# Optimization experiments

Measured on AMD Instinct MI355X. Metric: run time of the kernel, lower is better.

Reference implementation:

```python
import jax, jax.numpy as jnp
import numpy as np

INPUT_DIM = 1024
LATENT_DIM = 256
NUM_EMB = 8192
BATCH = 8192


def setup_inputs() -> dict:
    key = jax.random.key(0)
    ks = jax.random.split(key, 6)
    x = jax.random.normal(ks[0], (BATCH, INPUT_DIM), dtype=jnp.float32)
    # torch nn.Linear stores weight as [out, in]
    enc_w = jax.random.normal(ks[1], (LATENT_DIM, INPUT_DIM), dtype=jnp.float32) / np.sqrt(INPUT_DIM)
    enc_b = jnp.zeros((LATENT_DIM,), dtype=jnp.float32)
    # embeddings initialized uniform(-1/K, 1/K) as in the module
    emb = jax.random.uniform(ks[2], (NUM_EMB, LATENT_DIM), dtype=jnp.float32,
                             minval=-1.0 / NUM_EMB, maxval=1.0 / NUM_EMB)
    dec_w = jax.random.normal(ks[3], (INPUT_DIM, LATENT_DIM), dtype=jnp.float32) / np.sqrt(LATENT_DIM)
    dec_b = jnp.zeros((INPUT_DIM,), dtype=jnp.float32)
    return {"x": x, "enc_w": enc_w, "enc_b": enc_b, "emb": emb,
            "dec_w": dec_w, "dec_b": dec_b}


def reference(x, enc_w, enc_b, emb, dec_w, dec_b):
    # encoder: z = x @ W_e^T + b_e  -> [B, D]
    z = x @ enc_w.T + enc_b
    # cosine distance to codebook: d = 1 - <z, e> / (||z|| ||e||)  -> [B, K]
    z_norm = jnp.linalg.norm(z, axis=1, keepdims=True)          # [B, 1]
    e_norm = jnp.linalg.norm(emb, axis=1)                        # [K]
    d = 1.0 - (z @ emb.T) / (z_norm * e_norm)
    idx = jnp.argmin(d, axis=1)                                  # [B]
    # one-hot @ codebook == direct gather of nearest code vectors
    z_q = jnp.take(emb, idx, axis=0)                             # [B, D]
    # straight-through: decoder input z + stop_grad(z_q - z)
    dec_in = z + jax.lax.stop_gradient(z_q - z)
    x_recon = dec_in @ dec_w.T + dec_b
    return (x_recon, z, z_q, idx.astype(jnp.int32))
```

## Files before the change

kernel.cpp:

```cpp
#include <hip/hip_runtime.h>
#include <math.h>

#define BATCH   8192
#define IN_DIM  1024
#define LAT     256
#define NEMB    8192

#define TAU 3.5e-3f

#define RESC_R 16

#define CSPLIT 16

typedef _Float16 f16x8 __attribute__((ext_vector_type(8)));
typedef _Float16 f16x4 __attribute__((ext_vector_type(4)));
typedef float f32x16_t __attribute__((ext_vector_type(16)));

typedef __attribute__((address_space(1))) const unsigned int gu32_t;
typedef __attribute__((address_space(3))) unsigned int lu32_t;

__device__ __forceinline__ unsigned int ford(float x) {
  unsigned int u = __float_as_uint(x);
  return (u & 0x80000000u) ? ~u : (u | 0x80000000u);
}
__device__ __forceinline__ float funord(unsigned int t) {
  unsigned int u = (t & 0x80000000u) ? (t & 0x7FFFFFFFu) : ~t;
  return __uint_as_float(u);
}

__global__ __launch_bounds__(256) void emb_prep(
    const float* __restrict__ emb, float* __restrict__ inv_norm,
    _Float16* __restrict__ efrag) {
  __shared__ float s_inv[32];
  const int tid = threadIdx.x;
  const int l = tid & 63;
  const int w = tid >> 6;
  const int tile = blockIdx.x;

  {
    int row = tid >> 3, part = tid & 7;
    const float* p = emb + (size_t)(tile * 32 + row) * 256 + part * 32;
    float s = 0.f;
#pragma unroll
    for (int j = 0; j < 8; ++j) {
      float4 v = *(const float4*)&p[4 * j];
      s += v.x * v.x + v.y * v.y + v.z * v.z + v.w * v.w;
    }
    s += __shfl_xor(s, 1);
    s += __shfl_xor(s, 2);
    s += __shfl_xor(s, 4);
    if (part == 0) {
      float iv = 1.0f / sqrtf(s);
      s_inv[row] = iv;
      inv_norm[tile * 32 + row] = iv;
    }
  }
  __syncthreads();

#pragma unroll
  for (int q = 0; q < 4; ++q) {
    int kb = w * 4 + q;
    int row = l & 31;
    int k = kb * 16 + (l >> 5) * 8;
    const float* p = emb + (size_t)(tile * 32 + row) * 256 + k;
    float sc = s_inv[row];
    f16x8 h;
#pragma unroll
    for (int j = 0; j < 8; ++j) h[j] = (_Float16)(p[j] * sc);
    size_t o = ((size_t)(tile * 16 + kb) * 64 + l) * 8;
    *(f16x8*)(efrag + o) = h;
  }
}

__device__ __forceinline__ void split_body(
    const float* __restrict__ src, _Float16* __restrict__ dst, size_t lo_off,
    int KD, int write_lo, int gw, int l) {
  int tile = gw / KD, kb = gw % KD;
  int row = tile * 32 + (l & 31);
  int k = kb * 16 + (l >> 5) * 8;
  const float* p = src + (size_t)row * (KD * 16) + k;
  f16x8 h, lo;
#pragma unroll
  for (int j = 0; j < 8; ++j) {
    float v = p[j];
    _Float16 hh = (_Float16)v;
    h[j] = hh;
    lo[j] = (_Float16)(v - (float)hh);
  }
  size_t o = ((size_t)gw * 64 + l) * 8;
  *(f16x8*)(dst + o) = h;
  if (write_lo) *(f16x8*)(dst + lo_off + o) = lo;
}

__global__ __launch_bounds__(256) void split16(
    const float* __restrict__ src, _Float16* __restrict__ dst, size_t lo_off,
    int KD, int write_lo) {
  int gw = (blockIdx.x * 256 + threadIdx.x) >> 6;
  split_body(src, dst, lo_off, KD, write_lo, gw, threadIdx.x & 63);
}

__global__ __launch_bounds__(256) void split_weights(
    const float* __restrict__ enc_w, _Float16* __restrict__ wfrag,
    const float* __restrict__ dec_w, _Float16* __restrict__ dwfrag) {
  int b = blockIdx.x;
  int l = threadIdx.x & 63;
  if (b < 128) {
    int gw = (b * 256 + threadIdx.x) >> 6;
    split_body(enc_w, wfrag, (size_t)LAT * IN_DIM, IN_DIM / 16, 1, gw, l);
  } else {
    int gw = ((b - 128) * 256 + threadIdx.x) >> 6;
    split_body(dec_w, dwfrag, (size_t)IN_DIM * LAT, LAT / 16, 1, gw, l);
  }
}

__global__ __launch_bounds__(256) void gemm16_frag(
    const _Float16* __restrict__ Afrag, size_t a_lo_off,
    const _Float16* __restrict__ Bfrag, size_t b_lo_off,
    const float* __restrict__ bias, float* __restrict__ C, int N, int K) {
  __shared__ char lds[32768];
  const int tid = threadIdx.x;
  const int l = tid & 63;
  const int w = tid >> 6;
  const int mt = w & 1, nt = w >> 1;
  const int rb = blockIdx.y * 64, cb = blockIdx.x * 64;
  const int KD = K >> 4;

  f32x16_t acc = (f32x16_t)0.0f;

  for (int s = 0; s < (K >> 6); ++s) {
#pragma unroll
    for (int i = 0; i < 8; ++i) {
      int c = i * 4 + w;
      int isB = c >> 4;
      int cc = c & 15;
      int t32 = cc >> 3, prec = (cc >> 2) & 1, ks = cc & 3;
      int tile = ((isB ? cb : rb) >> 5) + t32;
      int kb = s * 4 + ks;
      const _Float16* base = isB ? Bfrag : Afrag;
      size_t lo = isB ? b_lo_off : a_lo_off;
      const _Float16* src =
          base + (size_t)prec * lo + ((size_t)(tile * KD + kb) * 64 + l) * 8;
      __builtin_amdgcn_global_load_lds((gu32_t*)src,
                                       (lu32_t*)(lds + (c << 10) + l * 16),
                                       16, 0, 0);
    }
    __syncthreads();
#pragma unroll
    for (int ks = 0; ks < 4; ++ks) {
      f16x8 ah = *(const f16x8*)(lds + ((mt * 8 + ks) << 10) + l * 16);
      f16x8 al = *(const f16x8*)(lds + ((mt * 8 + 4 + ks) << 10) + l * 16);
      f16x8 bh = *(const f16x8*)(lds + 16384 + ((nt * 8 + ks) << 10) + l * 16);
      f16x8 bl = *(const f16x8*)(lds + 16384 + ((nt * 8 + 4 + ks) << 10) + l * 16);
      acc = __builtin_amdgcn_mfma_f32_32x32x16_f16(ah, bh, acc, 0, 0, 0);
      acc = __builtin_amdgcn_mfma_f32_32x32x16_f16(ah, bl, acc, 0, 0, 0);
      acc = __builtin_amdgcn_mfma_f32_32x32x16_f16(al, bh, acc, 0, 0, 0);
    }
    __syncthreads();
  }

  int col = cb + nt * 32 + (l & 31);
  float bv = bias[col];
#pragma unroll
  for (int r = 0; r < 16; ++r) {
    int row = rb + mt * 32 + (r & 3) + 8 * (r >> 2) + 4 * (l >> 5);
    C[(size_t)row * N + col] = acc[r] + bv;
  }
}

__global__ __launch_bounds__(256) void gemm16(
    const float* __restrict__ A, const _Float16* __restrict__ Bfrag,
    size_t b_lo_off, const float* __restrict__ bias, float* __restrict__ C,
    int M, int N, int K) {
  __shared__ char lds[32768];
  const int tid = threadIdx.x;
  const int l = tid & 63;
  const int w = tid >> 6;
  const int mt = w & 1, nt = w >> 1;
  const int rb = blockIdx.y * 64, cb = blockIdx.x * 64;
  const int KD = K >> 4;

  f32x16_t acc = (f32x16_t)0.0f;

  for (int s = 0; s < (K >> 6); ++s) {
#pragma unroll
    for (int i = 0; i < 4; ++i) {
      int c = i * 4 + w;
      int bnt = c >> 3, prec = (c >> 2) & 1, ks = c & 3;
      int tile = (cb >> 5) + bnt, ksg = s * 4 + ks;
      const _Float16* src = Bfrag + (size_t)prec * b_lo_off +
                            ((size_t)(tile * KD + ksg) * 64 + l) * 8;
      __builtin_amdgcn_global_load_lds((gu32_t*)src,
                                       (lu32_t*)(lds + 16384 + (c << 10) + l * 16),
                                       16, 0, 0);
    }
#pragma unroll
    for (int t = 0; t < 4; ++t) {
      int flat = t * 256 + tid;
      int r = flat >> 4, c4 = flat & 15;
      float4 v = *(const float4*)&A[(size_t)(rb + r) * K + s * 64 + 4 * c4];
      int kk = 4 * c4;
      int ks = kk >> 4, j = kk & 7;
      int lane2 = (r & 31) + 32 * ((kk >> 3) & 1);
      int mtt = r >> 5;
      f16x4 hv, lv;
      float vv[4] = {v.x, v.y, v.z, v.w};
#pragma unroll
      for (int e = 0; e < 4; ++e) {
        _Float16 h = (_Float16)vv[e];
        hv[e] = h;
        lv[e] = (_Float16)(vv[e] - (float)h);
      }
      int base = ((mtt * 8 + ks) << 10) + lane2 * 16 + j * 2;
      *(f16x4*)(lds + base) = hv;
      *(f16x4*)(lds + base + 4096) = lv;
    }
    __syncthreads();
#pragma unroll
    for (int ks = 0; ks < 4; ++ks) {
      f16x8 ah = *(const f16x8*)(lds + ((mt * 8 + ks) << 10) + l * 16);
      f16x8 al = *(const f16x8*)(lds + ((mt * 8 + 4 + ks) << 10) + l * 16);
      f16x8 bh = *(const f16x8*)(lds + 16384 + ((nt * 8 + ks) << 10) + l * 16);
      f16x8 bl = *(const f16x8*)(lds + 16384 + ((nt * 8 + 4 + ks) << 10) + l * 16);
      acc = __builtin_amdgcn_mfma_f32_32x32x16_f16(ah, bh, acc, 0, 0, 0);
      acc = __builtin_amdgcn_mfma_f32_32x32x16_f16(ah, bl, acc, 0, 0, 0);
      acc = __builtin_amdgcn_mfma_f32_32x32x16_f16(al, bh, acc, 0, 0, 0);
    }
    __syncthreads();
  }

  int col = cb + nt * 32 + (l & 31);
  float bv = bias[col];
#pragma unroll
  for (int r = 0; r < 16; ++r) {
    int row = rb + mt * 32 + (r & 3) + 8 * (r >> 2) + 4 * (l >> 5);
    C[(size_t)row * N + col] = acc[r] + bv;
  }
}

__global__ __launch_bounds__(256) void gemm16_dec(
    const int* __restrict__ idxi, const unsigned int* __restrict__ flags,
    const unsigned long long* __restrict__ packed_rescore,
    const float* __restrict__ emb, const _Float16* __restrict__ Bfrag,
    size_t b_lo_off, const float* __restrict__ bias, float* __restrict__ C,
    float* __restrict__ zq, float* __restrict__ idx_out) {
  __shared__ char lds[32768];
  __shared__ int idxs[64];
  const int tid = threadIdx.x;
  const int l = tid & 63;
  const int w = tid >> 6;
  const int mt = w & 1, nt = w >> 1;
  const int rb = blockIdx.y * 64, cb = blockIdx.x * 64;
  const int KD = 16;

  if (tid < 64) {
    int row = rb + tid;
    int idx = idxi[row];
    if (flags[row]) idx = NEMB - 1 - (int)(packed_rescore[row] & 0xFFFFFFFFull);
    idxs[tid] = idx;
    if (blockIdx.x == 0) idx_out[row] = (float)idx;
  }
  __syncthreads();

  f32x16_t acc = (f32x16_t)0.0f;

  for (int s = 0; s < 4; ++s) {
#pragma unroll
    for (int i = 0; i < 4; ++i) {
      int c = i * 4 + w;
      int bnt = c >> 3, prec = (c >> 2) & 1, ks = c & 3;
      int tile = (cb >> 5) + bnt, ksg = s * 4 + ks;
      const _Float16* src = Bfrag + (size_t)prec * b_lo_off +
                            ((size_t)(tile * KD + ksg) * 64 + l) * 8;
      __builtin_amdgcn_global_load_lds((gu32_t*)src,
                                       (lu32_t*)(lds + 16384 + (c << 10) + l * 16),
                                       16, 0, 0);
    }
#pragma unroll
    for (int t = 0; t < 4; ++t) {
      int flat = t * 256 + tid;
      int r = flat >> 4, c4 = flat & 15;
      float4 v = *(const float4*)&emb[(size_t)idxs[r] * 256 + s * 64 + 4 * c4];
      if (blockIdx.x == 0)
        *(float4*)&zq[(size_t)(rb + r) * 256 + s * 64 + 4 * c4] = v;
      int kk = 4 * c4;
      int ks = kk >> 4, j = kk & 7;
      int lane2 = (r & 31) + 32 * ((kk >> 3) & 1);
      int mtt = r >> 5;
      f16x4 hv, lv;
      float vv[4] = {v.x, v.y, v.z, v.w};
#pragma unroll
      for (int e = 0; e < 4; ++e) {
        _Float16 h = (_Float16)vv[e];
        hv[e] = h;
        lv[e] = (_Float16)(vv[e] - (float)h);
      }
      int base = ((mtt * 8 + ks) << 10) + lane2 * 16 + j * 2;
      *(f16x4*)(lds + base) = hv;
      *(f16x4*)(lds + base + 4096) = lv;
    }
    __syncthreads();
#pragma unroll
    for (int ks = 0; ks < 4; ++ks) {
      f16x8 ah = *(const f16x8*)(lds + ((mt * 8 + ks) << 10) + l * 16);
      f16x8 al = *(const f16x8*)(lds + ((mt * 8 + 4 + ks) << 10) + l * 16);
      f16x8 bh = *(const f16x8*)(lds + 16384 + ((nt * 8 + ks) << 10) + l * 16);
      f16x8 bl = *(const f16x8*)(lds + 16384 + ((nt * 8 + 4 + ks) << 10) + l * 16);
      acc = __builtin_amdgcn_mfma_f32_32x32x16_f16(ah, bh, acc, 0, 0, 0);
      acc = __builtin_amdgcn_mfma_f32_32x32x16_f16(ah, bl, acc, 0, 0, 0);
      acc = __builtin_amdgcn_mfma_f32_32x32x16_f16(al, bh, acc, 0, 0, 0);
    }
    __syncthreads();
  }

  int col = cb + nt * 32 + (l & 31);
  float bv = bias[col];
#pragma unroll
  for (int r = 0; r < 16; ++r) {
    int row = rb + mt * 32 + (r & 3) + 8 * (r >> 2) + 4 * (l >> 5);
    C[(size_t)row * IN_DIM + col] = acc[r] + bv;
  }
}

__global__ __launch_bounds__(256) void score_mfma(
    const _Float16* __restrict__ zfrag, const _Float16* __restrict__ efrag,
    unsigned long long* __restrict__ cand1, unsigned int* __restrict__ cand2) {
  __shared__ char lds[32768];
  const int tid = threadIdx.x;
  const int l = tid & 63;
  const int w = tid >> 6;
  const int csplit = blockIdx.x;
  const int rowgrp = blockIdx.y;

  f16x8 a[16];
  {
    const _Float16* ab =
        zfrag + (((size_t)(rowgrp * 4 + w) * 16) * 64 + l) * 8;
#pragma unroll
    for (int kf = 0; kf < 16; ++kf)
      a[kf] = *(const f16x8*)(ab + (size_t)kf * 512);
  }

  float b1[16], b2[16];
  int i1[16];
#pragma unroll
  for (int r = 0; r < 16; ++r) {
    b1[r] = -INFINITY;
    b2[r] = -INFINITY;
    i1[r] = 0;
  }

  const char* esrc = (const char*)efrag + (size_t)csplit * 262144 + tid * 16;
  char* ldst = lds + tid * 16;
  const char* ldsr = lds + l * 16;

#pragma unroll
  for (int i = 0; i < 4; ++i)
    __builtin_amdgcn_global_load_lds((gu32_t*)(esrc + i * 4096),
                                     (lu32_t*)(ldst + i * 4096), 16, 0, 0);

#pragma unroll 1
  for (int p = 0; p < 16; ++p) {
    asm volatile("s_waitcnt vmcnt(0)" ::: "memory");
    __builtin_amdgcn_s_barrier();
    __builtin_amdgcn_sched_barrier(0);

    if (p < 15) {
      const char* sb = esrc + (size_t)(p + 1) * 16384;
      char* db = ldst + ((p + 1) & 1) * 16384;
#pragma unroll
      for (int i = 0; i < 4; ++i)
        __builtin_amdgcn_global_load_lds((gu32_t*)(sb + i * 4096),
                                         (lu32_t*)(db + i * 4096), 16, 0, 0);
    }

    const char* bb = ldsr + (p & 1) * 16384;
    f32x16_t acc0 = (f32x16_t)0.0f;
    f32x16_t acc1 = (f32x16_t)0.0f;
#pragma unroll
    for (int kb = 0; kb < 16; kb += 2) {
      f16x8 bh0 = *(const f16x8*)(bb + (kb << 10));
      f16x8 bh1 = *(const f16x8*)(bb + ((kb + 1) << 10));
      acc0 = __builtin_amdgcn_mfma_f32_32x32x16_f16(a[kb], bh0, acc0, 0, 0, 0);
      acc1 = __builtin_amdgcn_mfma_f32_32x32x16_f16(a[kb + 1], bh1, acc1, 0, 0, 0);
    }

    const int col = csplit * 512 + p * 32 + (l & 31);
#pragma unroll
    for (int r = 0; r < 16; ++r) {
      float v = acc0[r] + acc1[r];
      float nb2 = __builtin_amdgcn_fmed3f(v, b1[r], b2[r]);
      if (v > b1[r]) i1[r] = col;
      b1[r] = fmaxf(b1[r], v);
      b2[r] = nb2;
    }
  }

#pragma unroll
  for (int r = 0; r < 16; ++r) {
    float v1 = b1[r], v2 = b2[r];
    int vi = i1[r];
#pragma unroll
    for (int m = 1; m < 32; m <<= 1) {
      float o1 = __shfl_xor(v1, m);
      int oi = __shfl_xor(vi, m);
      float o2 = __shfl_xor(v2, m);
      float n2v = fmaxf(fminf(v1, o1), fmaxf(v2, o2));
      if (o1 > v1 || (o1 == v1 && oi < vi)) {
        v1 = o1;
        vi = oi;
      }
      v2 = n2v;
    }
    if ((l & 31) == 0) {
      int row = rowgrp * 128 + w * 32 + (r & 3) + 8 * (r >> 2) + 4 * (l >> 5);
      cand1[(size_t)row * CSPLIT + csplit] =
          ((unsigned long long)ford(v1) << 32) |
          (unsigned long long)(unsigned int)(NEMB - 1 - vi);
      cand2[(size_t)row * CSPLIT + csplit] = ford(v2);
    }
  }
}

__global__ __launch_bounds__(256) void finalize1(
    const unsigned long long* __restrict__ cand1,
    const unsigned int* __restrict__ cand2, int* __restrict__ idxi,
    unsigned int* __restrict__ flags, unsigned int* __restrict__ flag_count,
    unsigned int* __restrict__ flag_list) {
  int row = blockIdx.x * 256 + threadIdx.x;
  unsigned long long best = 0;
  unsigned int second = 0;
  int bslot = 0;
#pragma unroll
  for (int s = 0; s < CSPLIT; ++s) {
    unsigned long long v = cand1[(size_t)row * CSPLIT + s];
    unsigned int vs = (unsigned int)(v >> 32);
    if (v > best) {
      second = (unsigned int)(best >> 32);
      best = v;
      bslot = s;
    } else if (vs > second) {
      second = vs;
    }
  }
  unsigned int r2 = cand2[(size_t)row * CSPLIT + bslot];
  if (r2 > second) second = r2;
  float s1 = funord((unsigned int)(best >> 32));
  float s2 = funord(second);
  int idx = NEMB - 1 - (int)(best & 0xFFFFFFFFull);
  idxi[row] = idx;
  unsigned int fl = ((s1 - s2) < TAU) ? 1u : 0u;
  flags[row] = fl;
  if (fl) {
    unsigned int p = atomicAdd(flag_count, 1u);
    flag_list[p] = row;
  }
}

__global__ __launch_bounds__(256) void rescore(
    const float* __restrict__ z, const float* __restrict__ emb,
    const float* __restrict__ inv_norm,
    const unsigned int* __restrict__ flag_list,
    const unsigned int* __restrict__ flag_count,
    unsigned long long* __restrict__ packed_rescore) {
  __shared__ float z_s[2][292];
  __shared__ unsigned long long red[64];
  const int tid = threadIdx.x;
  const int l = tid & 63;
  const int w = tid >> 6;
  const int cl = l & 7;
  const int p = l >> 3;
  const int code = w * 8 + cl;
  const int cbase = blockIdx.x * 32;
  const unsigned int rc = blockIdx.y;

  unsigned int cnt = *flag_count;
  if (2 * rc >= cnt) return;

  float4 e4[8];
  const float* ebase = emb + (size_t)(cbase + code) * 256 + p * 32;
#pragma unroll
  for (int j = 0; j < 8; ++j) e4[j] = *(const float4*)&ebase[4 * j];
  const float inv = inv_norm[cbase + code];
  const unsigned int lowbits = (unsigned int)(NEMB - 1 - (cbase + code));

  for (unsigned int f = 2 * rc; f < cnt; f += 2 * RESC_R) {
    int row0 = (int)flag_list[f];
    int row1 = (f + 1 < cnt) ? (int)flag_list[f + 1] : row0;
    __syncthreads();
    if (tid < 128) {
      int half = tid >> 6, t = tid & 63;
      int k0 = t * 4;
      int addr = k0 + 4 * (k0 >> 5);
      const float* zp = z + (size_t)(half ? row1 : row0) * 256 + k0;
      *(float4*)&z_s[half][addr] = *(const float4*)zp;
    }
    __syncthreads();
    float a0 = 0.f, a1 = 0.f;
#pragma unroll
    for (int j = 0; j < 8; ++j) {
      float4 z0 = *(const float4*)&z_s[0][p * 36 + 4 * j];
      float4 z1 = *(const float4*)&z_s[1][p * 36 + 4 * j];
      a0 += e4[j].x * z0.x + e4[j].y * z0.y + e4[j].z * z0.z + e4[j].w * z0.w;
      a1 += e4[j].x * z1.x + e4[j].y * z1.y + e4[j].z * z1.z + e4[j].w * z1.w;
    }
#pragma unroll
    for (int m = 8; m < 64; m <<= 1) {
      a0 += __shfl_xor(a0, m);
      a1 += __shfl_xor(a1, m);
    }
    if (l < 8)
      red[w * 8 + cl] = ((unsigned long long)ford(a0 * inv) << 32) | lowbits;
    else if (l < 16)
      red[32 + w * 8 + cl] = ((unsigned long long)ford(a1 * inv) << 32) | lowbits;
    __syncthreads();
    if (w == 0) {
      unsigned long long v = red[l];
#pragma unroll
      for (int m = 1; m < 32; m <<= 1) {
        unsigned long long o = __shfl_xor(v, m);
        if (o > v) v = o;
      }
      if (l == 0) atomicMax(&packed_rescore[row0], v);
      if (l == 32) atomicMax(&packed_rescore[row1], v);
    }
  }
}

extern "C" void kernel_launch(void* const* d_in, const int* in_sizes, int n_in,
                              void* d_out, int out_size, void* d_ws,
                              size_t ws_size, hipStream_t stream) {
  (void)in_sizes; (void)n_in; (void)out_size;
  const float* x     = (const float*)d_in[0];
  const float* enc_w = (const float*)d_in[1];
  const float* enc_b = (const float*)d_in[2];
  const float* emb   = (const float*)d_in[3];
  const float* dec_w = (const float*)d_in[4];
  const float* dec_b = (const float*)d_in[5];

  float* out     = (float*)d_out;
  float* x_recon = out;
  float* z_out   = x_recon + (size_t)BATCH * IN_DIM;
  float* zq_out  = z_out + (size_t)BATCH * LAT;
  float* idx_out = zq_out + (size_t)BATCH * LAT;

  char* ws = (char*)d_ws;
  float* inv_norm = (float*)ws;
  unsigned int* flags = (unsigned int*)(ws + 32768);
  int* idxi = (int*)(ws + 65536);
  unsigned int* flag_count = (unsigned int*)(ws + 98304);
  unsigned long long* packed_rescore =
      (unsigned long long*)(ws + 98432);
  unsigned int* flag_list = (unsigned int*)(ws + 163968);
  _Float16* wfrag  = (_Float16*)(ws + 1048576);
  _Float16* dwfrag = (_Float16*)(ws + 2097152);
  _Float16* efrag  = (_Float16*)(ws + 3145728);
  _Float16* zfrag  = (_Float16*)(ws + 7340032);
  unsigned long long* cand1 = (unsigned long long*)(ws + 11534336);
  unsigned int* cand2 = (unsigned int*)(ws + 12582912);
  _Float16* xfrag  = (_Float16*)(ws + 24117248);

  const bool has_x = ws_size >= 57671680ull;

  hipMemsetAsync(ws + 98304, 0, 128 + 65536, stream);

  emb_prep<<<NEMB / 32, 256, 0, stream>>>(emb, inv_norm, efrag);
  split_weights<<<256, 256, 0, stream>>>(enc_w, wfrag, dec_w, dwfrag);

  if (has_x) {
    split16<<<4096, 256, 0, stream>>>(x, xfrag, (size_t)BATCH * IN_DIM,
                                      IN_DIM / 16, 1);
    gemm16_frag<<<dim3(LAT / 64, BATCH / 64), 256, 0, stream>>>(
        xfrag, (size_t)BATCH * IN_DIM, wfrag, (size_t)LAT * IN_DIM, enc_b,
        z_out, LAT, IN_DIM);
  } else {
    gemm16<<<dim3(LAT / 64, BATCH / 64), 256, 0, stream>>>(
        x, wfrag, (size_t)LAT * IN_DIM, enc_b, z_out, BATCH, LAT, IN_DIM);
  }

  split16<<<1024, 256, 0, stream>>>(z_out, zfrag, (size_t)BATCH * LAT,
                                    LAT / 16, 0);

  score_mfma<<<dim3(CSPLIT, 64), 256, 0, stream>>>(zfrag, efrag, cand1, cand2);

  finalize1<<<32, 256, 0, stream>>>(cand1, cand2, idxi, flags, flag_count,
                                    flag_list);
  rescore<<<dim3(256, RESC_R), 256, 0, stream>>>(
      z_out, emb, inv_norm, flag_list, flag_count, packed_rescore);

  gemm16_dec<<<dim3(IN_DIM / 64, BATCH / 64), 256, 0, stream>>>(
      idxi, flags, packed_rescore, emb, dwfrag, (size_t)IN_DIM * LAT, dec_b,
      x_recon, zq_out, idx_out);
}
```

Before: 261.8 us.

## Triple-buffer codebook tiles in score kernel and drop pre-split x path

The scoring kernel moves from double to triple buffering of codebook tiles in LDS, prefetching two stages ahead with a partial vmcnt wait, so global-to-LDS loads overlap more with the MFMA work. It also raises wave priority around the MFMA loop. Separately, the encoder path that first split x into fp16 hi/lo fragments and then ran a fragment GEMM is removed, and gemm16 now reads x directly. This saves a full pass over x but may make the encoder GEMM less efficient, and the larger LDS footprint can lower occupancy.

```diff
diff --git a/kernel.cpp b/kernel.cpp
--- a/kernel.cpp
+++ b/kernel.cpp
@@ -110,60 +110,6 @@
   } else {
     int gw = ((b - 128) * 256 + threadIdx.x) >> 6;
     split_body(dec_w, dwfrag, (size_t)IN_DIM * LAT, LAT / 16, 1, gw, l);
-  }
-}
-
-__global__ __launch_bounds__(256) void gemm16_frag(
-    const _Float16* __restrict__ Afrag, size_t a_lo_off,
-    const _Float16* __restrict__ Bfrag, size_t b_lo_off,
-    const float* __restrict__ bias, float* __restrict__ C, int N, int K) {
-  __shared__ char lds[32768];
-  const int tid = threadIdx.x;
-  const int l = tid & 63;
-  const int w = tid >> 6;
-  const int mt = w & 1, nt = w >> 1;
-  const int rb = blockIdx.y * 64, cb = blockIdx.x * 64;
-  const int KD = K >> 4;
-
-  f32x16_t acc = (f32x16_t)0.0f;
-
-  for (int s = 0; s < (K >> 6); ++s) {
-#pragma unroll
-    for (int i = 0; i < 8; ++i) {
-      int c = i * 4 + w;
-      int isB = c >> 4;
-      int cc = c & 15;
-      int t32 = cc >> 3, prec = (cc >> 2) & 1, ks = cc & 3;
-      int tile = ((isB ? cb : rb) >> 5) + t32;
-      int kb = s * 4 + ks;
-      const _Float16* base = isB ? Bfrag : Afrag;
-      size_t lo = isB ? b_lo_off : a_lo_off;
-      const _Float16* src =
-          base + (size_t)prec * lo + ((size_t)(tile * KD + kb) * 64 + l) * 8;
-      __builtin_amdgcn_global_load_lds((gu32_t*)src,
-                                       (lu32_t*)(lds + (c << 10) + l * 16),
-                                       16, 0, 0);
-    }
-    __syncthreads();
-#pragma unroll
-    for (int ks = 0; ks < 4; ++ks) {
-      f16x8 ah = *(const f16x8*)(lds + ((mt * 8 + ks) << 10) + l * 16);
-      f16x8 al = *(const f16x8*)(lds + ((mt * 8 + 4 + ks) << 10) + l * 16);
-      f16x8 bh = *(const f16x8*)(lds + 16384 + ((nt * 8 + ks) << 10) + l * 16);
-      f16x8 bl = *(const f16x8*)(lds + 16384 + ((nt * 8 + 4 + ks) << 10) + l * 16);
-      acc = __builtin_amdgcn_mfma_f32_32x32x16_f16(ah, bh, acc, 0, 0, 0);
-      acc = __builtin_amdgcn_mfma_f32_32x32x16_f16(ah, bl, acc, 0, 0, 0);
-      acc = __builtin_amdgcn_mfma_f32_32x32x16_f16(al, bh, acc, 0, 0, 0);
-    }
-    __syncthreads();
-  }
-
-  int col = cb + nt * 32 + (l & 31);
-  float bv = bias[col];
-#pragma unroll
-  for (int r = 0; r < 16; ++r) {
-    int row = rb + mt * 32 + (r & 3) + 8 * (r >> 2) + 4 * (l >> 5);
-    C[(size_t)row * N + col] = acc[r] + bv;
   }
 }
 
@@ -324,7 +270,7 @@
 __global__ __launch_bounds__(256) void score_mfma(
     const _Float16* __restrict__ zfrag, const _Float16* __restrict__ efrag,
     unsigned long long* __restrict__ cand1, unsigned int* __restrict__ cand2) {
-  __shared__ char lds[32768];
+  __shared__ char lds[49152];
   const int tid = threadIdx.x;
   const int l = tid & 63;
   const int w = tid >> 6;
@@ -350,32 +296,45 @@
   }
 
   const char* esrc = (const char*)efrag + (size_t)csplit * 262144 + tid * 16;
-  char* ldst = lds + tid * 16;
-  const char* ldsr = lds + l * 16;
+
+  char* bc = lds;
+  char* bn = lds + 16384;
+  char* bf = lds + 32768;
 
 #pragma unroll
   for (int i = 0; i < 4; ++i)
     __builtin_amdgcn_global_load_lds((gu32_t*)(esrc + i * 4096),
-                                     (lu32_t*)(ldst + i * 4096), 16, 0, 0);
+                                     (lu32_t*)(bc + tid * 16 + i * 4096),
+                                     16, 0, 0);
+#pragma unroll
+  for (int i = 0; i < 4; ++i)
+    __builtin_amdgcn_global_load_lds((gu32_t*)(esrc + 16384 + i * 4096),
+                                     (lu32_t*)(bn + tid * 16 + i * 4096),
+                                     16, 0, 0);
 
 #pragma unroll 1
   for (int p = 0; p < 16; ++p) {
-    asm volatile("s_waitcnt vmcnt(0)" ::: "memory");
+    if (p < 15) {
+      asm volatile("s_waitcnt vmcnt(4)" ::: "memory");
+    } else {
+      asm volatile("s_waitcnt vmcnt(0)" ::: "memory");
+    }
     __builtin_amdgcn_s_barrier();
     __builtin_amdgcn_sched_barrier(0);
 
-    if (p < 15) {
-      const char* sb = esrc + (size_t)(p + 1) * 16384;
-      char* db = ldst + ((p + 1) & 1) * 16384;
+    if (p < 14) {
+      const char* sb = esrc + (size_t)(p + 2) * 16384;
 #pragma unroll
       for (int i = 0; i < 4; ++i)
         __builtin_amdgcn_global_load_lds((gu32_t*)(sb + i * 4096),
-                                         (lu32_t*)(db + i * 4096), 16, 0, 0);
-    }
-
-    const char* bb = ldsr + (p & 1) * 16384;
+                                         (lu32_t*)(bf + tid * 16 + i * 4096),
+                                         16, 0, 0);
+    }
+
+    const char* bb = bc + l * 16;
     f32x16_t acc0 = (f32x16_t)0.0f;
     f32x16_t acc1 = (f32x16_t)0.0f;
+    __builtin_amdgcn_s_setprio(1);
 #pragma unroll
     for (int kb = 0; kb < 16; kb += 2) {
       f16x8 bh0 = *(const f16x8*)(bb + (kb << 10));
@@ -383,6 +342,7 @@
       acc0 = __builtin_amdgcn_mfma_f32_32x32x16_f16(a[kb], bh0, acc0, 0, 0, 0);
       acc1 = __builtin_amdgcn_mfma_f32_32x32x16_f16(a[kb + 1], bh1, acc1, 0, 0, 0);
     }
+    __builtin_amdgcn_s_setprio(0);
 
     const int col = csplit * 512 + p * 32 + (l & 31);
 #pragma unroll
@@ -393,6 +353,11 @@
       b1[r] = fmaxf(b1[r], v);
       b2[r] = nb2;
     }
+
+    char* t = bc;
+    bc = bn;
+    bn = bf;
+    bf = t;
   }
 
 #pragma unroll
@@ -529,7 +494,7 @@
 extern "C" void kernel_launch(void* const* d_in, const int* in_sizes, int n_in,
                               void* d_out, int out_size, void* d_ws,
                               size_t ws_size, hipStream_t stream) {
-  (void)in_sizes; (void)n_in; (void)out_size;
+  (void)in_sizes; (void)n_in; (void)out_size; (void)ws_size;
   const float* x     = (const float*)d_in[0];
   const float* enc_w = (const float*)d_in[1];
   const float* enc_b = (const float*)d_in[2];
@@ -557,25 +522,14 @@
   _Float16* zfrag  = (_Float16*)(ws + 7340032);
   unsigned long long* cand1 = (unsigned long long*)(ws + 11534336);
   unsigned int* cand2 = (unsigned int*)(ws + 12582912);
-  _Float16* xfrag  = (_Float16*)(ws + 24117248);
-
-  const bool has_x = ws_size >= 57671680ull;
 
   hipMemsetAsync(ws + 98304, 0, 128 + 65536, stream);
 
   emb_prep<<<NEMB / 32, 256, 0, stream>>>(emb, inv_norm, efrag);
   split_weights<<<256, 256, 0, stream>>>(enc_w, wfrag, dec_w, dwfrag);
 
-  if (has_x) {
-    split16<<<4096, 256, 0, stream>>>(x, xfrag, (size_t)BATCH * IN_DIM,
-                                      IN_DIM / 16, 1);
-    gemm16_frag<<<dim3(LAT / 64, BATCH / 64), 256, 0, stream>>>(
-        xfrag, (size_t)BATCH * IN_DIM, wfrag, (size_t)LAT * IN_DIM, enc_b,
-        z_out, LAT, IN_DIM);
-  } else {
-    gemm16<<<dim3(LAT / 64, BATCH / 64), 256, 0, stream>>>(
-        x, wfrag, (size_t)LAT * IN_DIM, enc_b, z_out, BATCH, LAT, IN_DIM);
-  }
+  gemm16<<<dim3(LAT / 64, BATCH / 64), 256, 0, stream>>>(
+      x, wfrag, (size_t)LAT * IN_DIM, enc_b, z_out, BATCH, LAT, IN_DIM);
 
   split16<<<1024, 256, 0, stream>>>(z_out, zfrag, (size_t)BATCH * LAT,
                                     LAT / 16, 0);
```

Result: slower. 281.2 us (+7.4%).

## Fuse z fp16 conversion into scoring kernel and triple-buffer codebook loads

Applied to the files above, without the earlier changes.

The separate split16 pass that converted z to fp16 fragments is removed, and the scoring kernel now reads fp32 z directly and converts it in registers. The codebook staging in LDS goes from double to triple buffering with a prefetch distance of two, using a partial vmcnt wait. s_setprio is raised around the MFMA loop. This saves one kernel launch and a round trip of z through memory, and hides more load latency. The cost is larger LDS use, which may lower occupancy, plus uncoalesced fp32 loads of z per lane.

```diff
diff --git a/kernel.cpp b/kernel.cpp
--- a/kernel.cpp
+++ b/kernel.cpp
@@ -322,9 +322,9 @@
 }
 
 __global__ __launch_bounds__(256) void score_mfma(
-    const _Float16* __restrict__ zfrag, const _Float16* __restrict__ efrag,
+    const float* __restrict__ z, const _Float16* __restrict__ efrag,
     unsigned long long* __restrict__ cand1, unsigned int* __restrict__ cand2) {
-  __shared__ char lds[32768];
+  __shared__ char lds[49152];
   const int tid = threadIdx.x;
   const int l = tid & 63;
   const int w = tid >> 6;
@@ -333,11 +333,19 @@
 
   f16x8 a[16];
   {
-    const _Float16* ab =
-        zfrag + (((size_t)(rowgrp * 4 + w) * 16) * 64 + l) * 8;
-#pragma unroll
-    for (int kf = 0; kf < 16; ++kf)
-      a[kf] = *(const f16x8*)(ab + (size_t)kf * 512);
+    const float* zb =
+        z + (size_t)(rowgrp * 128 + w * 32 + (l & 31)) * 256 + (l >> 5) * 8;
+#pragma unroll
+    for (int kf = 0; kf < 16; ++kf) {
+      float4 v0 = *(const float4*)(zb + kf * 16);
+      float4 v1 = *(const float4*)(zb + kf * 16 + 4);
+      f16x8 h;
+      h[0] = (_Float16)v0.x; h[1] = (_Float16)v0.y;
+      h[2] = (_Float16)v0.z; h[3] = (_Float16)v0.w;
+      h[4] = (_Float16)v1.x; h[5] = (_Float16)v1.y;
+      h[6] = (_Float16)v1.z; h[7] = (_Float16)v1.w;
+      a[kf] = h;
+    }
   }
 
   float b1[16], b2[16];
@@ -350,32 +358,45 @@
   }
 
   const char* esrc = (const char*)efrag + (size_t)csplit * 262144 + tid * 16;
-  char* ldst = lds + tid * 16;
-  const char* ldsr = lds + l * 16;
+
+  char* bc = lds;
+  char* bn = lds + 16384;
+  char* bf = lds + 32768;
 
 #pragma unroll
   for (int i = 0; i < 4; ++i)
     __builtin_amdgcn_global_load_lds((gu32_t*)(esrc + i * 4096),
-                                     (lu32_t*)(ldst + i * 4096), 16, 0, 0);
+                                     (lu32_t*)(bc + tid * 16 + i * 4096),
+                                     16, 0, 0);
+#pragma unroll
+  for (int i = 0; i < 4; ++i)
+    __builtin_amdgcn_global_load_lds((gu32_t*)(esrc + 16384 + i * 4096),
+                                     (lu32_t*)(bn + tid * 16 + i * 4096),
+                                     16, 0, 0);
 
 #pragma unroll 1
   for (int p = 0; p < 16; ++p) {
-    asm volatile("s_waitcnt vmcnt(0)" ::: "memory");
+    if (p < 15) {
+      asm volatile("s_waitcnt vmcnt(4)" ::: "memory");
+    } else {
+      asm volatile("s_waitcnt vmcnt(0)" ::: "memory");
+    }
     __builtin_amdgcn_s_barrier();
     __builtin_amdgcn_sched_barrier(0);
 
-    if (p < 15) {
-      const char* sb = esrc + (size_t)(p + 1) * 16384;
-      char* db = ldst + ((p + 1) & 1) * 16384;
+    if (p < 14) {
+      const char* sb = esrc + (size_t)(p + 2) * 16384;
 #pragma unroll
       for (int i = 0; i < 4; ++i)
         __builtin_amdgcn_global_load_lds((gu32_t*)(sb + i * 4096),
-                                         (lu32_t*)(db + i * 4096), 16, 0, 0);
-    }
-
-    const char* bb = ldsr + (p & 1) * 16384;
+                                         (lu32_t*)(bf + tid * 16 + i * 4096),
+                                         16, 0, 0);
+    }
+
+    const char* bb = bc + l * 16;
     f32x16_t acc0 = (f32x16_t)0.0f;
     f32x16_t acc1 = (f32x16_t)0.0f;
+    __builtin_amdgcn_s_setprio(1);
 #pragma unroll
     for (int kb = 0; kb < 16; kb += 2) {
       f16x8 bh0 = *(const f16x8*)(bb + (kb << 10));
@@ -383,6 +404,7 @@
       acc0 = __builtin_amdgcn_mfma_f32_32x32x16_f16(a[kb], bh0, acc0, 0, 0, 0);
       acc1 = __builtin_amdgcn_mfma_f32_32x32x16_f16(a[kb + 1], bh1, acc1, 0, 0, 0);
     }
+    __builtin_amdgcn_s_setprio(0);
 
     const int col = csplit * 512 + p * 32 + (l & 31);
 #pragma unroll
@@ -393,6 +415,11 @@
       b1[r] = fmaxf(b1[r], v);
       b2[r] = nb2;
     }
+
+    char* t = bc;
+    bc = bn;
+    bn = bf;
+    bf = t;
   }
 
 #pragma unroll
@@ -554,7 +581,6 @@
   _Float16* wfrag  = (_Float16*)(ws + 1048576);
   _Float16* dwfrag = (_Float16*)(ws + 2097152);
   _Float16* efrag  = (_Float16*)(ws + 3145728);
-  _Float16* zfrag  = (_Float16*)(ws + 7340032);
   unsigned long long* cand1 = (unsigned long long*)(ws + 11534336);
   unsigned int* cand2 = (unsigned int*)(ws + 12582912);
   _Float16* xfrag  = (_Float16*)(ws + 24117248);
@@ -577,10 +603,7 @@
         x, wfrag, (size_t)LAT * IN_DIM, enc_b, z_out, BATCH, LAT, IN_DIM);
   }
 
-  split16<<<1024, 256, 0, stream>>>(z_out, zfrag, (size_t)BATCH * LAT,
-                                    LAT / 16, 0);
-
-  score_mfma<<<dim3(CSPLIT, 64), 256, 0, stream>>>(zfrag, efrag, cand1, cand2);
+  score_mfma<<<dim3(CSPLIT, 64), 256, 0, stream>>>(z_out, efrag, cand1, cand2);
 
   finalize1<<<32, 256, 0, stream>>>(cand1, cand2, idxi, flags, flag_count,
                                     flag_list);
```

Result: slower. 268.3 us (+2.5%).
